# Kernel tuning notes

Hardware: AMD Instinct MI355X
Metric: run time of the kernel (lower is better)

Reference implementation:

```python
import jax, jax.numpy as jnp
import numpy as np

B, T, IN, H = 4096, 2048, 3, 4

def setup_inputs() -> dict:
    key = jax.random.key(0)
    k1, k2, k3, k4, k5 = jax.random.split(key, 5)
    s_ih = 1.0 / np.sqrt(H)
    return {
        "x": jax.random.normal(k1, (B, T, IN), dtype=jnp.float32),
        # PyTorch LSTM weights, gate order (i, f, g, o), no bias
        "w_ih": jax.random.uniform(k2, (4 * H, IN), dtype=jnp.float32, minval=-s_ih, maxval=s_ih),
        "w_hh": jax.random.uniform(k3, (4 * H, H), dtype=jnp.float32, minval=-s_ih, maxval=s_ih),
        "fc_w": jax.random.uniform(k4, (1, H), dtype=jnp.float32, minval=-0.5, maxval=0.5),
        "fc_b": jax.random.uniform(k5, (1,), dtype=jnp.float32, minval=-0.5, maxval=0.5),
    }

def reference(x, w_ih, w_hh, fc_w, fc_b):
    b = x.shape[0]
    # Precompute input projections for all timesteps in one GEMM: [T, B, 4H]
    xt = jnp.swapaxes(x, 0, 1)                      # [T, B, IN]
    x_proj = jnp.einsum('tbi,gi->tbg', xt, w_ih)    # [T, B, 4H]

    def step(carry, xp):
        h, c = carry
        gates = xp + h @ w_hh.T                     # [B, 4H]
        i, f, g, o = jnp.split(gates, 4, axis=-1)
        i = jax.nn.sigmoid(i)
        f = jax.nn.sigmoid(f)
        g = jnp.tanh(g)
        o = jax.nn.sigmoid(o)
        c = f * c + i * g
        h = o * jnp.tanh(c)
        return (h, c), None

    h0 = jnp.zeros((b, H), dtype=x.dtype)
    c0 = jnp.zeros((b, H), dtype=x.dtype)
    (h_last, _), _ = jax.lax.scan(step, (h0, c0), x_proj)
    # out[:, -1, :] of the LSTM outputs is exactly the final hidden state
    return h_last @ fc_w.T + fc_b                   # [B, 1]
```

## Files before the change

kernel.cpp:

```cpp
#include <hip/hip_runtime.h>


static constexpr int T_STEPS = 2048;
static constexpr int CHUNK   = 16;
static constexpr int NCHUNK  = T_STEPS / CHUNK;

template<int CTRL>
__device__ __forceinline__ float dpp_f(float v) {
    return __int_as_float(__builtin_amdgcn_update_dpp(
        0, __float_as_int(v), CTRL, 0xF, 0xF, false));
}

struct Ctx {
    float wih0, wih1, wih2;
    float whh0, whh1, whh2, whh3;
    float m, Aa, Bb;
    bool  b0, b1fo;
};

template<int J>
__device__ __forceinline__ float comp(const float4& v) {
    if constexpr (J == 0) return v.x;
    else if constexpr (J == 1) return v.y;
    else if constexpr (J == 2) return v.z;
    else return v.w;
}

template<int TT>
__device__ __forceinline__ void projx_t(float (&xp)[CHUNK], const float4 (&bf)[12],
                                        const Ctx& k) {
    constexpr int j0 = 3 * TT, j1 = j0 + 1, j2 = j0 + 2;
    float x0 = comp<(j0 & 3)>(bf[j0 >> 2]);
    float x1 = comp<(j1 & 3)>(bf[j1 >> 2]);
    float x2 = comp<(j2 & 3)>(bf[j2 >> 2]);
    xp[TT] = fmaf(x0, k.wih0, fmaf(x1, k.wih1, x2 * k.wih2));
    if constexpr (TT + 1 < CHUNK) projx_t<TT + 1>(xp, bf, k);
}

__device__ __forceinline__ void lstm_step(float xp, float& h, float& c, const Ctx& k) {
    float hb0 = dpp_f<0x00>(h);
    float hb1 = dpp_f<0x55>(h);
    float hb2 = dpp_f<0xAA>(h);
    float hb3 = dpp_f<0xFF>(h);

    float p0 = fmaf(hb1, k.whh1, fmaf(hb0, k.whh0, xp));
    float p1 = fmaf(hb2, k.whh2, hb3 * k.whh3);
    float gp = p0 + p1;

    float e   = __builtin_amdgcn_exp2f(k.m * gp);
    float act = fmaf(k.Aa, __builtin_amdgcn_rcpf(1.0f + e), k.Bb);

    float t1 = dpp_f<0x124>(act);
    float t2 = dpp_f<0x128>(act);
    float t3 = dpp_f<0x12C>(act);
    float prod = k.b0 ? t1 * t3 : act * t2;
    float A  = k.b0 ? t2  : t1;
    float Bv = k.b0 ? act : t3;
    float f  = k.b1fo ? A : Bv;
    float o  = k.b1fo ? Bv : A;

    float cn = fmaf(f, c, prod);
    c = cn;
    float e2 = __builtin_amdgcn_exp2f(-2.885390081777927f * cn);
    float th = fmaf(2.0f, __builtin_amdgcn_rcpf(1.0f + e2), -1.0f);
    h = o * th;
}

template<int TT>
__device__ __forceinline__ void steps16(const float (&xp)[CHUNK], float& h, float& c,
                                        const Ctx& k) {
    lstm_step(xp[TT], h, c, k);
    if constexpr (TT + 1 < CHUNK) steps16<TT + 1>(xp, h, c, k);
}

__device__ __forceinline__ void loadbf(float4 (&bf)[12], const float4* p) {
    #pragma unroll
    for (int i = 0; i < 12; ++i) bf[i] = p[i];
}

__global__ __launch_bounds__(256, 1) void lstm_kernel(
    const float* __restrict__ x,
    const float* __restrict__ w_ih,
    const float* __restrict__ w_hh,
    const float* __restrict__ fc_w,
    const float* __restrict__ fc_b,
    float* __restrict__ out)
{
    const int tid = threadIdx.x;
    const int l16 = tid & 15;
    const int b   = blockIdx.x * 16 + (tid >> 4);
    const int gt  = l16 >> 2;

    Ctx k;
    k.wih0 = w_ih[l16 * 3 + 0];
    k.wih1 = w_ih[l16 * 3 + 1];
    k.wih2 = w_ih[l16 * 3 + 2];
    k.whh0 = w_hh[l16 * 4 + 0];
    k.whh1 = w_hh[l16 * 4 + 1];
    k.whh2 = w_hh[l16 * 4 + 2];
    k.whh3 = w_hh[l16 * 4 + 3];
    const bool is_g = (gt == 2);
    k.m  = is_g ? -2.885390081777927f : -1.4426950408889634f;
    k.Aa = is_g ? 2.0f : 1.0f;
    k.Bb = is_g ? -1.0f : 0.0f;
    k.b0 = (gt & 1) != 0;

    {
        float probe = (float)l16;
        float t1p = dpp_f<0x124>(probe);
        bool dirB = (t1p == (float)((l16 + 4) & 15));
        k.b1fo = (((gt & 2) != 0) != dirB);
    }

    const float4* xb4 = reinterpret_cast<const float4*>(x + (size_t)b * (T_STEPS * 3));

    float4 bfA[12], bfB[12];
    float  xpA[CHUNK], xpB[CHUNK];
    loadbf(bfA, xb4);
    loadbf(bfB, xb4 + 12);
    projx_t<0>(xpA, bfA, k);

    float h = 0.f, c = 0.f;

    for (int it = 0; it < NCHUNK / 2; ++it) {
        const int ca = (2 * it + 2 < NCHUNK) ? 2 * it + 2 : NCHUNK - 1;
        loadbf(bfA, xb4 + ca * 12);
        projx_t<0>(xpB, bfB, k);
        steps16<0>(xpA, h, c, k);
        const int cb = (2 * it + 3 < NCHUNK) ? 2 * it + 3 : NCHUNK - 1;
        loadbf(bfB, xb4 + cb * 12);
        projx_t<0>(xpA, bfA, k);
        steps16<0>(xpB, h, c, k);
    }

    float r = h * fc_w[l16 & 3];
    r += dpp_f<0xB1>(r);
    r += dpp_f<0x4E>(r);
    if (l16 == 0) out[b] = r + fc_b[0];
}

extern "C" void kernel_launch(void* const* d_in, const int* in_sizes, int n_in,
                              void* d_out, int out_size, void* d_ws, size_t ws_size,
                              hipStream_t stream) {
    const float* x    = (const float*)d_in[0];
    const float* w_ih = (const float*)d_in[1];
    const float* w_hh = (const float*)d_in[2];
    const float* fc_w = (const float*)d_in[3];
    const float* fc_b = (const float*)d_in[4];
    float* out = (float*)d_out;

    dim3 grid(4096 / 16);
    dim3 block(256);
    hipLaunchKernelGGL(lstm_kernel, grid, block, 0, stream,
                       x, w_ih, w_hh, fc_w, fc_b, out);
}
```

Before: 204.9 us.

## Interleave two independent batch recurrences per thread and fold exp scale into weights

Each 16-lane group now runs two batch elements, interleaving their LSTM steps so the two independent dependency chains can hide each other's latency. The grid is halved to 128 blocks, and the chunk size drops to 8 to keep register use in check. The sigmoid/tanh exp2 scale factor is pre-multiplied into w_ih and w_hh, which removes one multiply per step. The cost is half as many blocks (128, fewer than the GPU's CUs) and more registers per thread.

```diff
diff --git a/kernel.cpp b/kernel.cpp
--- a/kernel.cpp
+++ b/kernel.cpp
@@ -2,7 +2,7 @@
 
 
 static constexpr int T_STEPS = 2048;
-static constexpr int CHUNK   = 16;
+static constexpr int CHUNK   = 8;
 static constexpr int NCHUNK  = T_STEPS / CHUNK;
 
 template<int CTRL>
@@ -14,7 +14,7 @@
 struct Ctx {
     float wih0, wih1, wih2;
     float whh0, whh1, whh2, whh3;
-    float m, Aa, Bb;
+    float Aa, Bb;
     bool  b0, b1fo;
 };
 
@@ -27,14 +27,14 @@
 }
 
 template<int TT>
-__device__ __forceinline__ void projx_t(float (&xp)[CHUNK], const float4 (&bf)[12],
-                                        const Ctx& k) {
+__device__ __forceinline__ void projx8(float (&xp)[CHUNK], const float4 (&bf)[6],
+                                       const Ctx& k) {
     constexpr int j0 = 3 * TT, j1 = j0 + 1, j2 = j0 + 2;
     float x0 = comp<(j0 & 3)>(bf[j0 >> 2]);
     float x1 = comp<(j1 & 3)>(bf[j1 >> 2]);
     float x2 = comp<(j2 & 3)>(bf[j2 >> 2]);
     xp[TT] = fmaf(x0, k.wih0, fmaf(x1, k.wih1, x2 * k.wih2));
-    if constexpr (TT + 1 < CHUNK) projx_t<TT + 1>(xp, bf, k);
+    if constexpr (TT + 1 < CHUNK) projx8<TT + 1>(xp, bf, k);
 }
 
 __device__ __forceinline__ void lstm_step(float xp, float& h, float& c, const Ctx& k) {
@@ -47,7 +47,7 @@
     float p1 = fmaf(hb2, k.whh2, hb3 * k.whh3);
     float gp = p0 + p1;
 
-    float e   = __builtin_amdgcn_exp2f(k.m * gp);
+    float e   = __builtin_amdgcn_exp2f(gp);
     float act = fmaf(k.Aa, __builtin_amdgcn_rcpf(1.0f + e), k.Bb);
 
     float t1 = dpp_f<0x124>(act);
@@ -67,15 +67,17 @@
 }
 
 template<int TT>
-__device__ __forceinline__ void steps16(const float (&xp)[CHUNK], float& h, float& c,
-                                        const Ctx& k) {
-    lstm_step(xp[TT], h, c, k);
-    if constexpr (TT + 1 < CHUNK) steps16<TT + 1>(xp, h, c, k);
+__device__ __forceinline__ void steps2(const float (&xpA)[CHUNK], const float (&xpB)[CHUNK],
+                                       float& hA, float& cA, float& hB, float& cB,
+                                       const Ctx& k) {
+    lstm_step(xpA[TT], hA, cA, k);
+    lstm_step(xpB[TT], hB, cB, k);
+    if constexpr (TT + 1 < CHUNK) steps2<TT + 1>(xpA, xpB, hA, cA, hB, cB, k);
 }
 
-__device__ __forceinline__ void loadbf(float4 (&bf)[12], const float4* p) {
+__device__ __forceinline__ void loadbf6(float4 (&bf)[6], const float4* p) {
     #pragma unroll
-    for (int i = 0; i < 12; ++i) bf[i] = p[i];
+    for (int i = 0; i < 6; ++i) bf[i] = p[i];
 }
 
 __global__ __launch_bounds__(256, 1) void lstm_kernel(
@@ -88,23 +90,24 @@
 {
     const int tid = threadIdx.x;
     const int l16 = tid & 15;
-    const int b   = blockIdx.x * 16 + (tid >> 4);
+    const int pr  = blockIdx.x * 16 + (tid >> 4);
+    const int b0  = 2 * pr, b1 = 2 * pr + 1;
     const int gt  = l16 >> 2;
 
+    const bool is_g = (gt == 2);
+    const float mm  = is_g ? -2.885390081777927f : -1.4426950408889634f;
+
     Ctx k;
-    k.wih0 = w_ih[l16 * 3 + 0];
-    k.wih1 = w_ih[l16 * 3 + 1];
-    k.wih2 = w_ih[l16 * 3 + 2];
-    k.whh0 = w_hh[l16 * 4 + 0];
-    k.whh1 = w_hh[l16 * 4 + 1];
-    k.whh2 = w_hh[l16 * 4 + 2];
-    k.whh3 = w_hh[l16 * 4 + 3];
-    const bool is_g = (gt == 2);
-    k.m  = is_g ? -2.885390081777927f : -1.4426950408889634f;
+    k.wih0 = mm * w_ih[l16 * 3 + 0];
+    k.wih1 = mm * w_ih[l16 * 3 + 1];
+    k.wih2 = mm * w_ih[l16 * 3 + 2];
+    k.whh0 = mm * w_hh[l16 * 4 + 0];
+    k.whh1 = mm * w_hh[l16 * 4 + 1];
+    k.whh2 = mm * w_hh[l16 * 4 + 2];
+    k.whh3 = mm * w_hh[l16 * 4 + 3];
     k.Aa = is_g ? 2.0f : 1.0f;
     k.Bb = is_g ? -1.0f : 0.0f;
     k.b0 = (gt & 1) != 0;
-
     {
         float probe = (float)l16;
         float t1p = dpp_f<0x124>(probe);
@@ -112,31 +115,47 @@
         k.b1fo = (((gt & 2) != 0) != dirB);
     }
 
-    const float4* xb4 = reinterpret_cast<const float4*>(x + (size_t)b * (T_STEPS * 3));
+    const float4* xA = reinterpret_cast<const float4*>(x + (size_t)b0 * (T_STEPS * 3));
+    const float4* xB = reinterpret_cast<const float4*>(x + (size_t)b1 * (T_STEPS * 3));
 
-    float4 bfA[12], bfB[12];
-    float  xpA[CHUNK], xpB[CHUNK];
-    loadbf(bfA, xb4);
-    loadbf(bfB, xb4 + 12);
-    projx_t<0>(xpA, bfA, k);
+    float4 bfA0[6], bfA1[6], bfB0[6], bfB1[6];
+    float  xpA0[CHUNK], xpA1[CHUNK], xpB0[CHUNK], xpB1[CHUNK];
 
-    float h = 0.f, c = 0.f;
+    loadbf6(bfA0, xA);      loadbf6(bfA1, xB);
+    loadbf6(bfB0, xA + 6);  loadbf6(bfB1, xB + 6);
+    projx8<0>(xpA0, bfA0, k);
+    projx8<0>(xpA1, bfA1, k);
+
+    float hA = 0.f, cA = 0.f, hB = 0.f, cB = 0.f;
 
     for (int it = 0; it < NCHUNK / 2; ++it) {
         const int ca = (2 * it + 2 < NCHUNK) ? 2 * it + 2 : NCHUNK - 1;
-        loadbf(bfA, xb4 + ca * 12);
-        projx_t<0>(xpB, bfB, k);
-        steps16<0>(xpA, h, c, k);
+        loadbf6(bfA0, xA + ca * 6);
+        loadbf6(bfA1, xB + ca * 6);
+        projx8<0>(xpB0, bfB0, k);
+        projx8<0>(xpB1, bfB1, k);
+        steps2<0>(xpA0, xpA1, hA, cA, hB, cB, k);
+
         const int cb = (2 * it + 3 < NCHUNK) ? 2 * it + 3 : NCHUNK - 1;
-        loadbf(bfB, xb4 + cb * 12);
-        projx_t<0>(xpA, bfA, k);
-        steps16<0>(xpB, h, c, k);
+        loadbf6(bfB0, xA + cb * 6);
+        loadbf6(bfB1, xB + cb * 6);
+        projx8<0>(xpA0, bfA0, k);
+        projx8<0>(xpA1, bfA1, k);
+        steps2<0>(xpB0, xpB1, hA, cA, hB, cB, k);
     }
 
-    float r = h * fc_w[l16 & 3];
-    r += dpp_f<0xB1>(r);
-    r += dpp_f<0x4E>(r);
-    if (l16 == 0) out[b] = r + fc_b[0];
+    const float fw = fc_w[l16 & 3];
+    float rA = hA * fw;
+    rA += dpp_f<0xB1>(rA);
+    rA += dpp_f<0x4E>(rA);
+    float rB = hB * fw;
+    rB += dpp_f<0xB1>(rB);
+    rB += dpp_f<0x4E>(rB);
+    if (l16 == 0) {
+        const float fcb = fc_b[0];
+        out[b0] = rA + fcb;
+        out[b1] = rB + fcb;
+    }
 }
 
 extern "C" void kernel_launch(void* const* d_in, const int* in_sizes, int n_in,
@@ -149,7 +168,7 @@
     const float* fc_b = (const float*)d_in[4];
     float* out = (float*)d_out;
 
-    dim3 grid(4096 / 16);
+    dim3 grid(4096 / 32);
     dim3 block(256);
     hipLaunchKernelGGL(lstm_kernel, grid, block, 0, stream,
                        x, w_ih, w_hh, fc_w, fc_b, out);
```

New measurement: 365.6 us. 78.4% more time.
